# Performance work log

Measured on AMD Instinct MI355X. Metric: run time of the kernel, lower is better.

## Reference

```python
import jax, jax.numpy as jnp
import numpy as np

B, H, M, N, D = 8, 8, 512, 512, 64
HID = 16
MIX1 = (1.0 / 2.0) ** 0.5
MIX2 = (1.0 / 16.0) ** 0.5


def setup_inputs() -> dict:
    key = jax.random.key(0)
    ks = jax.random.split(key, 8)
    q = jax.random.normal(ks[0], (B, H, M, D), dtype=jnp.float32)
    k = jax.random.normal(ks[1], (B, H, N, D), dtype=jnp.float32)
    v = jax.random.normal(ks[2], (B, H, N, D), dtype=jnp.float32)
    dmat = jax.random.uniform(ks[3], (B, M, N), dtype=jnp.float32)
    mix_W1 = jax.random.uniform(ks[4], (H, 2, HID), minval=-MIX1, maxval=MIX1, dtype=jnp.float32)
    mix_b1 = jax.random.uniform(ks[5], (H, HID), minval=-MIX1, maxval=MIX1, dtype=jnp.float32)
    mix_W2 = jax.random.uniform(ks[6], (H, HID, 1), minval=-MIX2, maxval=MIX2, dtype=jnp.float32)
    mix_b2 = jax.random.uniform(ks[7], (H, 1), minval=-MIX2, maxval=MIX2, dtype=jnp.float32)
    return {"q": q, "k": k, "v": v, "dmat": dmat,
            "mix_W1": mix_W1, "mix_b1": mix_b1, "mix_W2": mix_W2, "mix_b2": mix_b2}


def reference(q, k, v, dmat, mix_W1, mix_b1, mix_W2, mix_b2):
    # attention scores: [b,h,m,n]
    scale = 1.0 / jnp.sqrt(jnp.float32(k.shape[-1]))
    scores = jnp.einsum("bhmd,bhnd->bhmn", q, k) * scale
    # stack dot-product scores with distance matrix: [b,h,m,n,2]
    mixed = jnp.stack([scores, jnp.broadcast_to(dmat[:, None, :, :], scores.shape)], axis=-1)
    # per-head 2-layer MLP over the 2-channel axis
    h1 = jax.nn.relu(jnp.einsum("bhmnc,hcf->bhmnf", mixed, mix_W1)
                     + mix_b1[None, :, None, None, :])          # [b,h,m,n,HID]
    mixed_scores = (jnp.einsum("bhmnf,hfo->bhmno", h1, mix_W2)[..., 0]
                    + mix_b2[None, :, None, None, 0])            # [b,h,m,n]
    attn = jax.nn.softmax(mixed_scores, axis=-1)
    return jnp.einsum("bhmn,bhnd->bhmd", attn, v)
```

## Files before the change

kernel.cpp:

```cpp
#include <hip/hip_runtime.h>
#include <hip/hip_bf16.h>


typedef __attribute__((ext_vector_type(4))) float f32x4;
typedef __attribute__((ext_vector_type(8))) __bf16 bf16x8;
typedef __attribute__((ext_vector_type(4))) __bf16 bf16x4;

static __device__ __forceinline__ float rlf(float x) {
    return __uint_as_float(__builtin_amdgcn_readfirstlane(__float_as_uint(x)));
}
static __device__ __forceinline__ void cvt2(float x, __bf16& h, __bf16& l) {
    h = (__bf16)x;
    l = (__bf16)(x - (float)h);
}
static __device__ __forceinline__ int sw64(int row, int col) {
    return row * 64 + ((((col >> 3) ^ (row & 7)) << 3) | (col & 7));
}
static __device__ __forceinline__ void dma16(const __bf16* g, __bf16* l) {
    __builtin_amdgcn_global_load_lds(
        (const __attribute__((address_space(1))) unsigned*)g,
        (__attribute__((address_space(3))) unsigned*)l, 16, 0, 0);
}

#define B_ 8
#define H_ 8
#define M_ 512
#define N_ 512
#define D_ 64
#define HID_ 16

__global__ __launch_bounds__(256) void prep_kernel(
    const float* __restrict__ kg, const float* __restrict__ vg,
    __bf16* __restrict__ ws)
{
    __shared__ float vld[64 * 68];
    const int t   = threadIdx.x;
    const int blk = blockIdx.x;
    const long base = (long)blk * 4096;
    __bf16* out = ws + (long)blk * 16384;

#pragma unroll
    for (int it = 0; it < 4; ++it) {
        const int e = it * 1024 + t * 4;
        const int rr = e >> 6, c0 = e & 63;
        f32x4 v4 = *(const f32x4*)(vg + base + e);
        *(f32x4*)(vld + rr * 68 + c0) = v4;
    }

#pragma unroll
    for (int qq = t; qq < 512; qq += 256) {
        const int row = qq >> 3, c = qq & 7;
        const float* src = kg + base + row * 64 + ((c ^ (row & 7)) << 3);
        f32x4 a = *(const f32x4*)src;
        f32x4 b4 = *(const f32x4*)(src + 4);
        bf16x8 hv, lv;
#pragma unroll
        for (int j = 0; j < 4; ++j) {
            __bf16 h, l;
            cvt2(a[j], h, l);  hv[j] = h;     lv[j] = l;
            cvt2(b4[j], h, l); hv[4 + j] = h; lv[4 + j] = l;
        }
        *(bf16x8*)(out + qq * 8) = hv;
        *(bf16x8*)(out + 4096 + qq * 8) = lv;
    }
    __syncthreads();

#pragma unroll
    for (int qq = t; qq < 512; qq += 256) {
        const int d = qq & 63, c = qq >> 6;
        bf16x8 hv, lv;
#pragma unroll
        for (int j = 0; j < 8; ++j) {
            const int n = ((c ^ (d & 7)) << 3) + j;
            __bf16 h, l;
            cvt2(vld[n * 68 + d], h, l);
            hv[j] = h; lv[j] = l;
        }
        const int pos = d * 64 + c * 8;
        *(bf16x8*)(out + 8192 + pos) = hv;
        *(bf16x8*)(out + 12288 + pos) = lv;
    }
}

__global__ __launch_bounds__(256, 2) void msdpa_kernel(
    const float* __restrict__ qg, const __bf16* __restrict__ ws,
    const float* __restrict__ dg, const float* __restrict__ w1g,
    const float* __restrict__ b1g, const float* __restrict__ w2g,
    float* __restrict__ outg)
{
    extern __shared__ __bf16 smem[];

    const int tid  = threadIdx.x;
    const int lane = tid & 63;
    const int wv   = tid >> 6;
    const int r16  = lane & 15;
    const int g    = lane >> 4;

    const int bm = blockIdx.x;
    const int h  = blockIdx.y;
    const int b  = blockIdx.z;

    __bf16* PHw = smem + 32768 + wv * 1024;
    __bf16* PLw = smem + 36864 + wv * 1024;

    const long bh = (long)(b * H_ + h);
    const __bf16* wsbh = ws + bh * (8L * 16384);
    const float* dmp = dg + ((long)b * M_ + (long)bm * 64 + wv * 16 + r16) * N_ + g * 4;

    __bf16* bcur = smem;
    __bf16* bnxt = smem + 16384;

#pragma unroll
    for (int i = 0; i < 8; ++i)
        dma16(wsbh + i * 2048 + tid * 8, bcur + i * 2048 + tid * 8);

    const float* w1h = w1g + h * 2 * HID_;
    const float* b1h = b1g + h * HID_;
    const float* w2h = w2g + h * HID_;
    float af[HID_], cf[HID_], bf_[HID_], wa[HID_];
    float A = 0.f, C = 0.f, B0 = 0.f;
#pragma unroll
    for (int f = 0; f < HID_; ++f) {
        af[f] = rlf(w1h[f]) * 0.125f;
        cf[f] = rlf(w1h[HID_ + f]);
        bf_[f] = rlf(b1h[f]);
        wa[f] = rlf(w2h[f]) * (1.4426950408889634f * 0.5f);
        A  = fmaf(wa[f], af[f], A);
        C  = fmaf(wa[f], cf[f], C);
        B0 = fmaf(wa[f], bf_[f], B0);
    }

    const float* qbase = qg + (bh * M_ + (long)bm * 64 + wv * 16 + r16) * D_;
    bf16x8 qh[2], ql[2];
#pragma unroll
    for (int ks = 0; ks < 2; ++ks) {
        f32x4 x0 = *(const f32x4*)(qbase + ks * 32 + g * 8);
        f32x4 x1 = *(const f32x4*)(qbase + ks * 32 + g * 8 + 4);
        bf16x8 hv, lv;
#pragma unroll
        for (int j = 0; j < 4; ++j) {
            __bf16 h_, l_;
            cvt2(x0[j], h_, l_); hv[j] = h_; lv[j] = l_;
            cvt2(x1[j], h_, l_); hv[4 + j] = h_; lv[4 + j] = l_;
        }
        qh[ks] = hv; ql[ks] = lv;
    }

    f32x4 dmvc[4], dmvn[4];
#pragma unroll
    for (int n16 = 0; n16 < 4; ++n16)
        dmvc[n16] = *(const f32x4*)(dmp + n16 * 16);

    f32x4 oacc[4];
#pragma unroll
    for (int dt = 0; dt < 4; ++dt) oacc[dt] = f32x4{0.f, 0.f, 0.f, 0.f};
    float mrun = -1e30f, lsum = 0.0f;

    __syncthreads();

    for (int nt = 0; nt < 8; ++nt) {
        if (nt < 7) {
            const __bf16* tile = wsbh + (nt + 1) * 16384;
#pragma unroll
            for (int i = 0; i < 8; ++i)
                dma16(tile + i * 2048 + tid * 8, bnxt + i * 2048 + tid * 8);
#pragma unroll
            for (int n16 = 0; n16 < 4; ++n16)
                dmvn[n16] = *(const f32x4*)(dmp + (nt + 1) * 64 + n16 * 16);
        }

        __bf16* KH  = bcur;
        __bf16* KL  = bcur + 4096;
        __bf16* VTH = bcur + 8192;
        __bf16* VTL = bcur + 12288;

        f32x4 sacc[4];
#pragma unroll
        for (int n16 = 0; n16 < 4; ++n16) sacc[n16] = f32x4{0.f, 0.f, 0.f, 0.f};
#pragma unroll
        for (int n16 = 0; n16 < 4; ++n16) {
            const int row = n16 * 16 + r16;
#pragma unroll
            for (int ks = 0; ks < 2; ++ks) {
                const int off = sw64(row, ks * 32 + g * 8);
                bf16x8 kh_ = *(const bf16x8*)(KH + off);
                bf16x8 kl_ = *(const bf16x8*)(KL + off);
                sacc[n16] = __builtin_amdgcn_mfma_f32_16x16x32_bf16(kh_, qh[ks], sacc[n16], 0, 0, 0);
                sacc[n16] = __builtin_amdgcn_mfma_f32_16x16x32_bf16(kh_, ql[ks], sacc[n16], 0, 0, 0);
                sacc[n16] = __builtin_amdgcn_mfma_f32_16x16x32_bf16(kl_, qh[ks], sacc[n16], 0, 0, 0);
            }
        }

        float ms[4][4];
#pragma unroll
        for (int n16 = 0; n16 < 4; ++n16)
#pragma unroll
            for (int r = 0; r < 4; ++r) {
                const float s = sacc[n16][r], d = dmvc[n16][r];
                float acc = fmaf(A, s, fmaf(C, d, B0));
#pragma unroll
                for (int f = 0; f < HID_; ++f) {
                    const float u = fmaf(af[f], s, fmaf(cf[f], d, bf_[f]));
                    acc = fmaf(wa[f], fabsf(u), acc);
                }
                ms[n16][r] = acc;
            }

        float mloc = -1e30f;
#pragma unroll
        for (int n16 = 0; n16 < 4; ++n16)
#pragma unroll
            for (int r = 0; r < 4; ++r) mloc = fmaxf(mloc, ms[n16][r]);
        mloc = fmaxf(mloc, __shfl_xor(mloc, 16));
        mloc = fmaxf(mloc, __shfl_xor(mloc, 32));
        const float mnew = fmaxf(mrun, mloc);
        const float sc = exp2f(mrun - mnew);
        mrun = mnew;

        float psum = 0.0f;
#pragma unroll
        for (int n16 = 0; n16 < 4; ++n16) {
            bf16x4 ph4, pl4;
#pragma unroll
            for (int r = 0; r < 4; ++r) {
                const float p = exp2f(ms[n16][r] - mnew);
                psum += p;
                __bf16 h_, l_;
                cvt2(p, h_, l_);
                ph4[r] = h_; pl4[r] = l_;
            }
            const int cc = 2 * n16 + (g >> 1);
            const int pos = r16 * 64 + (((cc ^ (r16 & 7)) << 3) | ((g & 1) << 2));
            *(bf16x4*)(PHw + pos) = ph4;
            *(bf16x4*)(PLw + pos) = pl4;
        }
        lsum = lsum * sc + psum;

        float scm[4];
#pragma unroll
        for (int r = 0; r < 4; ++r) scm[r] = __shfl(sc, g * 4 + r);
#pragma unroll
        for (int dt = 0; dt < 4; ++dt)
#pragma unroll
            for (int r = 0; r < 4; ++r) oacc[dt][r] *= scm[r];

#pragma unroll
        for (int ks = 0; ks < 2; ++ks) {
            const int pofs = r16 * 64 + ((((ks * 4 + g)) ^ (r16 & 7)) << 3);
            bf16x8 pa = *(const bf16x8*)(PHw + pofs);
            bf16x8 pb = *(const bf16x8*)(PLw + pofs);
#pragma unroll
            for (int dt = 0; dt < 4; ++dt) {
                const int vofs = sw64(dt * 16 + r16, ks * 32 + g * 8);
                bf16x8 vh = *(const bf16x8*)(VTH + vofs);
                bf16x8 vl = *(const bf16x8*)(VTL + vofs);
                oacc[dt] = __builtin_amdgcn_mfma_f32_16x16x32_bf16(pa, vh, oacc[dt], 0, 0, 0);
                oacc[dt] = __builtin_amdgcn_mfma_f32_16x16x32_bf16(pa, vl, oacc[dt], 0, 0, 0);
                oacc[dt] = __builtin_amdgcn_mfma_f32_16x16x32_bf16(pb, vh, oacc[dt], 0, 0, 0);
            }
        }

        if (nt < 7) {
            __syncthreads();
            __bf16* tmp = bcur; bcur = bnxt; bnxt = tmp;
#pragma unroll
            for (int n16 = 0; n16 < 4; ++n16) dmvc[n16] = dmvn[n16];
        }
    }

    lsum += __shfl_xor(lsum, 16);
    lsum += __shfl_xor(lsum, 32);
    float linv[4];
#pragma unroll
    for (int r = 0; r < 4; ++r) linv[r] = 1.0f / __shfl(lsum, g * 4 + r);

    float* obase = outg + (bh * M_ + (long)bm * 64 + wv * 16) * D_;
#pragma unroll
    for (int dt = 0; dt < 4; ++dt)
#pragma unroll
        for (int r = 0; r < 4; ++r)
            obase[(g * 4 + r) * D_ + dt * 16 + r16] = oacc[dt][r] * linv[r];
}

extern "C" void kernel_launch(void* const* d_in, const int* in_sizes, int n_in,
                              void* d_out, int out_size, void* d_ws, size_t ws_size,
                              hipStream_t stream) {
    const float* q  = (const float*)d_in[0];
    const float* k  = (const float*)d_in[1];
    const float* v  = (const float*)d_in[2];
    const float* dm = (const float*)d_in[3];
    const float* w1 = (const float*)d_in[4];
    const float* b1 = (const float*)d_in[5];
    const float* w2 = (const float*)d_in[6];
    float* out = (float*)d_out;
    __bf16* ws = (__bf16*)d_ws;

    prep_kernel<<<dim3(512), dim3(256), 0, stream>>>(k, v, ws);

    (void)hipFuncSetAttribute(reinterpret_cast<const void*>(msdpa_kernel),
                              hipFuncAttributeMaxDynamicSharedMemorySize, 81920);
    dim3 grid(M_ / 64, H_, B_);
    msdpa_kernel<<<grid, dim3(256), 81920, stream>>>(q, ws, dm, w1, b1, w2, out);
}
```

Baseline: 133.2 us.

## Split key tile across two wave groups per block with cross-wave softmax merge

Doubles the block to 512 threads so each 64-key tile is split between two groups of four waves, each handling 32 keys for the same 16 query rows. Row maxima are exchanged through shared memory, and the partial outputs and sums are merged at the end. The V transpose swizzle is changed so P can stay in registers as the MFMA A operand, which removes the P staging round-trip through LDS. The aim is to halve the per-thread work on the costly MLP epilogue and raise wave-level parallelism. In exchange it adds an extra block barrier per tile and a final reduction through shared memory.

```diff
diff --git a/kernel.cpp b/kernel.cpp
--- a/kernel.cpp
+++ b/kernel.cpp
@@ -70,11 +70,14 @@
         const int d = qq & 63, c = qq >> 6;
         bf16x8 hv, lv;
 #pragma unroll
-        for (int j = 0; j < 8; ++j) {
-            const int n = ((c ^ (d & 7)) << 3) + j;
-            __bf16 h, l;
-            cvt2(vld[n * 68 + d], h, l);
-            hv[j] = h; lv[j] = l;
+        for (int dd = 0; dd < 2; ++dd) {
+            const int nb = (((2 * c + dd) ^ (d & 15)) << 2);
+#pragma unroll
+            for (int jj = 0; jj < 4; ++jj) {
+                __bf16 h, l;
+                cvt2(vld[(nb + jj) * 68 + d], h, l);
+                hv[dd * 4 + jj] = h; lv[dd * 4 + jj] = l;
+            }
         }
         const int pos = d * 64 + c * 8;
         *(bf16x8*)(out + 8192 + pos) = hv;
@@ -82,37 +85,37 @@
     }
 }
 
-__global__ __launch_bounds__(256, 2) void msdpa_kernel(
+__global__ __launch_bounds__(512, 4) void msdpa_kernel(
     const float* __restrict__ qg, const __bf16* __restrict__ ws,
     const float* __restrict__ dg, const float* __restrict__ w1g,
     const float* __restrict__ b1g, const float* __restrict__ w2g,
     float* __restrict__ outg)
 {
     extern __shared__ __bf16 smem[];
+    float* xm  = (float*)(smem + 32768);
+    float* xls = xm + 128;
 
     const int tid  = threadIdx.x;
     const int lane = tid & 63;
     const int wv   = tid >> 6;
     const int r16  = lane & 15;
     const int g    = lane >> 4;
+    const int rw   = wv & 3;
+    const int hn   = wv >> 2;
 
     const int bm = blockIdx.x;
     const int h  = blockIdx.y;
     const int b  = blockIdx.z;
 
-    __bf16* PHw = smem + 32768 + wv * 1024;
-    __bf16* PLw = smem + 36864 + wv * 1024;
-
     const long bh = (long)(b * H_ + h);
     const __bf16* wsbh = ws + bh * (8L * 16384);
-    const float* dmp = dg + ((long)b * M_ + (long)bm * 64 + wv * 16 + r16) * N_ + g * 4;
 
     __bf16* bcur = smem;
     __bf16* bnxt = smem + 16384;
 
 #pragma unroll
-    for (int i = 0; i < 8; ++i)
-        dma16(wsbh + i * 2048 + tid * 8, bcur + i * 2048 + tid * 8);
+    for (int i = 0; i < 4; ++i)
+        dma16(wsbh + i * 4096 + tid * 8, bcur + i * 4096 + tid * 8);
 
     const float* w1h = w1g + h * 2 * HID_;
     const float* b1h = b1g + h * HID_;
@@ -130,7 +133,7 @@
         B0 = fmaf(wa[f], bf_[f], B0);
     }
 
-    const float* qbase = qg + (bh * M_ + (long)bm * 64 + wv * 16 + r16) * D_;
+    const float* qbase = qg + (bh * M_ + (long)bm * 64 + rw * 16 + r16) * D_;
     bf16x8 qh[2], ql[2];
 #pragma unroll
     for (int ks = 0; ks < 2; ++ks) {
@@ -146,9 +149,11 @@
         qh[ks] = hv; ql[ks] = lv;
     }
 
-    f32x4 dmvc[4], dmvn[4];
-#pragma unroll
-    for (int n16 = 0; n16 < 4; ++n16)
+    const float* dmp = dg + ((long)b * M_ + (long)bm * 64 + rw * 16 + r16) * N_
+                          + hn * 32 + g * 4;
+    f32x4 dmvc[2], dmvn[2];
+#pragma unroll
+    for (int n16 = 0; n16 < 2; ++n16)
         dmvc[n16] = *(const f32x4*)(dmp + n16 * 16);
 
     f32x4 oacc[4];
@@ -162,10 +167,10 @@
         if (nt < 7) {
             const __bf16* tile = wsbh + (nt + 1) * 16384;
 #pragma unroll
-            for (int i = 0; i < 8; ++i)
-                dma16(tile + i * 2048 + tid * 8, bnxt + i * 2048 + tid * 8);
-#pragma unroll
-            for (int n16 = 0; n16 < 4; ++n16)
+            for (int i = 0; i < 4; ++i)
+                dma16(tile + i * 4096 + tid * 8, bnxt + i * 4096 + tid * 8);
+#pragma unroll
+            for (int n16 = 0; n16 < 2; ++n16)
                 dmvn[n16] = *(const f32x4*)(dmp + (nt + 1) * 64 + n16 * 16);
         }
 
@@ -174,12 +179,12 @@
         __bf16* VTH = bcur + 8192;
         __bf16* VTL = bcur + 12288;
 
-        f32x4 sacc[4];
-#pragma unroll
-        for (int n16 = 0; n16 < 4; ++n16) sacc[n16] = f32x4{0.f, 0.f, 0.f, 0.f};
-#pragma unroll
-        for (int n16 = 0; n16 < 4; ++n16) {
-            const int row = n16 * 16 + r16;
+        f32x4 sacc[2];
+#pragma unroll
+        for (int n16 = 0; n16 < 2; ++n16) sacc[n16] = f32x4{0.f, 0.f, 0.f, 0.f};
+#pragma unroll
+        for (int n16 = 0; n16 < 2; ++n16) {
+            const int row = hn * 32 + n16 * 16 + r16;
 #pragma unroll
             for (int ks = 0; ks < 2; ++ks) {
                 const int off = sw64(row, ks * 32 + g * 8);
@@ -191,9 +196,9 @@
             }
         }
 
-        float ms[4][4];
-#pragma unroll
-        for (int n16 = 0; n16 < 4; ++n16)
+        float ms[2][4];
+#pragma unroll
+        for (int n16 = 0; n16 < 2; ++n16)
 #pragma unroll
             for (int r = 0; r < 4; ++r) {
                 const float s = sacc[n16][r], d = dmvc[n16][r];
@@ -206,80 +211,94 @@
                 ms[n16][r] = acc;
             }
 
-        float mloc = -1e30f;
-#pragma unroll
-        for (int n16 = 0; n16 < 4; ++n16)
-#pragma unroll
-            for (int r = 0; r < 4; ++r) mloc = fmaxf(mloc, ms[n16][r]);
+        float mloc = fmaxf(fmaxf(fmaxf(ms[0][0], ms[0][1]), fmaxf(ms[0][2], ms[0][3])),
+                           fmaxf(fmaxf(ms[1][0], ms[1][1]), fmaxf(ms[1][2], ms[1][3])));
         mloc = fmaxf(mloc, __shfl_xor(mloc, 16));
         mloc = fmaxf(mloc, __shfl_xor(mloc, 32));
-        const float mnew = fmaxf(mrun, mloc);
-        const float sc = exp2f(mrun - mnew);
+        float p[8], psum = 0.f;
+#pragma unroll
+        for (int n16 = 0; n16 < 2; ++n16)
+#pragma unroll
+            for (int r = 0; r < 4; ++r) {
+                const float pv = exp2f(ms[n16][r] - mloc);
+                p[n16 * 4 + r] = pv;
+                psum += pv;
+            }
+        if (g == 0) xm[wv * 16 + r16] = mloc;
+        __syncthreads();
+
+        const float mloc2 = xm[(wv ^ 4) * 16 + r16];
+        const float mnew = fmaxf(mrun, fmaxf(mloc, mloc2));
+        const float scO  = exp2f(mrun - mnew);
+        const float fac1 = exp2f(mloc - mnew);
         mrun = mnew;
-
-        float psum = 0.0f;
-#pragma unroll
-        for (int n16 = 0; n16 < 4; ++n16) {
-            bf16x4 ph4, pl4;
-#pragma unroll
-            for (int r = 0; r < 4; ++r) {
-                const float p = exp2f(ms[n16][r] - mnew);
-                psum += p;
-                __bf16 h_, l_;
-                cvt2(p, h_, l_);
-                ph4[r] = h_; pl4[r] = l_;
-            }
-            const int cc = 2 * n16 + (g >> 1);
-            const int pos = r16 * 64 + (((cc ^ (r16 & 7)) << 3) | ((g & 1) << 2));
-            *(bf16x4*)(PHw + pos) = ph4;
-            *(bf16x4*)(PLw + pos) = pl4;
-        }
-        lsum = lsum * sc + psum;
+        lsum = fmaf(lsum, scO, psum * fac1);
+
+        bf16x8 pa, pb;
+#pragma unroll
+        for (int j = 0; j < 8; ++j) {
+            __bf16 h_, l_;
+            cvt2(p[j] * fac1, h_, l_);
+            pa[j] = h_; pb[j] = l_;
+        }
 
         float scm[4];
 #pragma unroll
-        for (int r = 0; r < 4; ++r) scm[r] = __shfl(sc, g * 4 + r);
+        for (int r = 0; r < 4; ++r) scm[r] = __shfl(scO, g * 4 + r);
 #pragma unroll
         for (int dt = 0; dt < 4; ++dt)
 #pragma unroll
             for (int r = 0; r < 4; ++r) oacc[dt][r] *= scm[r];
 
 #pragma unroll
-        for (int ks = 0; ks < 2; ++ks) {
-            const int pofs = r16 * 64 + ((((ks * 4 + g)) ^ (r16 & 7)) << 3);
-            bf16x8 pa = *(const bf16x8*)(PHw + pofs);
-            bf16x8 pb = *(const bf16x8*)(PLw + pofs);
-#pragma unroll
-            for (int dt = 0; dt < 4; ++dt) {
-                const int vofs = sw64(dt * 16 + r16, ks * 32 + g * 8);
-                bf16x8 vh = *(const bf16x8*)(VTH + vofs);
-                bf16x8 vl = *(const bf16x8*)(VTL + vofs);
-                oacc[dt] = __builtin_amdgcn_mfma_f32_16x16x32_bf16(pa, vh, oacc[dt], 0, 0, 0);
-                oacc[dt] = __builtin_amdgcn_mfma_f32_16x16x32_bf16(pa, vl, oacc[dt], 0, 0, 0);
-                oacc[dt] = __builtin_amdgcn_mfma_f32_16x16x32_bf16(pb, vh, oacc[dt], 0, 0, 0);
-            }
-        }
-
-        if (nt < 7) {
-            __syncthreads();
-            __bf16* tmp = bcur; bcur = bnxt; bnxt = tmp;
-#pragma unroll
-            for (int n16 = 0; n16 < 4; ++n16) dmvc[n16] = dmvn[n16];
-        }
+        for (int dt = 0; dt < 4; ++dt) {
+            const int rowb = (dt * 16 + r16) * 64;
+            const int p0 = ((hn * 8 + g) ^ r16) * 4;
+            const int p1 = ((hn * 8 + 4 + g) ^ r16) * 4;
+            bf16x4 vh0 = *(const bf16x4*)(VTH + rowb + p0);
+            bf16x4 vh1 = *(const bf16x4*)(VTH + rowb + p1);
+            bf16x4 vl0 = *(const bf16x4*)(VTL + rowb + p0);
+            bf16x4 vl1 = *(const bf16x4*)(VTL + rowb + p1);
+            bf16x8 vh = __builtin_shufflevector(vh0, vh1, 0, 1, 2, 3, 4, 5, 6, 7);
+            bf16x8 vl = __builtin_shufflevector(vl0, vl1, 0, 1, 2, 3, 4, 5, 6, 7);
+            oacc[dt] = __builtin_amdgcn_mfma_f32_16x16x32_bf16(pa, vh, oacc[dt], 0, 0, 0);
+            oacc[dt] = __builtin_amdgcn_mfma_f32_16x16x32_bf16(pa, vl, oacc[dt], 0, 0, 0);
+            oacc[dt] = __builtin_amdgcn_mfma_f32_16x16x32_bf16(pb, vh, oacc[dt], 0, 0, 0);
+        }
+
+        __syncthreads();
+        __bf16* tmp = bcur; bcur = bnxt; bnxt = tmp;
+#pragma unroll
+        for (int n16 = 0; n16 < 2; ++n16) dmvc[n16] = dmvn[n16];
     }
 
     lsum += __shfl_xor(lsum, 16);
     lsum += __shfl_xor(lsum, 32);
-    float linv[4];
-#pragma unroll
-    for (int r = 0; r < 4; ++r) linv[r] = 1.0f / __shfl(lsum, g * 4 + r);
-
-    float* obase = outg + (bh * M_ + (long)bm * 64 + wv * 16) * D_;
-#pragma unroll
-    for (int dt = 0; dt < 4; ++dt)
-#pragma unroll
-        for (int r = 0; r < 4; ++r)
-            obase[(g * 4 + r) * D_ + dt * 16 + r16] = oacc[dt][r] * linv[r];
+
+    float* obuf = (float*)smem;
+    if (hn == 1) {
+        if (g == 0) xls[rw * 16 + r16] = lsum;
+#pragma unroll
+        for (int dt = 0; dt < 4; ++dt)
+#pragma unroll
+            for (int r = 0; r < 4; ++r)
+                obuf[rw * 1024 + (g * 4 + r) * 64 + dt * 16 + r16] = oacc[dt][r];
+    }
+    __syncthreads();
+    if (hn == 0) {
+        const float Ltot = lsum + xls[rw * 16 + r16];
+        float linv[4];
+#pragma unroll
+        for (int r = 0; r < 4; ++r) linv[r] = 1.0f / __shfl(Ltot, g * 4 + r);
+        float* obase = outg + (bh * M_ + (long)bm * 64 + rw * 16) * D_;
+#pragma unroll
+        for (int dt = 0; dt < 4; ++dt)
+#pragma unroll
+            for (int r = 0; r < 4; ++r) {
+                const float o2 = obuf[rw * 1024 + (g * 4 + r) * 64 + dt * 16 + r16];
+                obase[(g * 4 + r) * D_ + dt * 16 + r16] = (oacc[dt][r] + o2) * linv[r];
+            }
+    }
 }
 
 extern "C" void kernel_launch(void* const* d_in, const int* in_sizes, int n_in,
@@ -298,7 +317,7 @@
     prep_kernel<<<dim3(512), dim3(256), 0, stream>>>(k, v, ws);
 
     (void)hipFuncSetAttribute(reinterpret_cast<const void*>(msdpa_kernel),
-                              hipFuncAttributeMaxDynamicSharedMemorySize, 81920);
+                              hipFuncAttributeMaxDynamicSharedMemorySize, 66560);
     dim3 grid(M_ / 64, H_, B_);
-    msdpa_kernel<<<grid, dim3(256), 81920, stream>>>(q, ws, dm, w1, b1, w2, out);
-}
+    msdpa_kernel<<<grid, dim3(512), 66560, stream>>>(q, ws, dm, w1, b1, w2, out);
+}
```

Result: slower. 137.9 us (+3.5%).
